# Kernel tuning notes

Hardware: AMD Instinct MI355X
Metric: run time of the kernel (lower is better)

## Reference

```python
import jax, jax.numpy as jnp
import numpy as np

D_MODEL = 1024
N_HEADS = 16
N_GROUPS = 4
D_FF = 4096
N_EXPERTS = 8
TOP_K = 2
BATCH = 2
SEQ = 1024
D_K = D_MODEL // N_HEADS
HPG = N_HEADS // N_GROUPS
EPS = 1e-6


def rms_norm(x, w):
    rms = jnp.sqrt(jnp.mean(x * x, axis=-1, keepdims=True) + EPS)
    return x / rms * w


def rope(x):
    # RoPE over FULL d_model, halves concatenated (faithful to source quirk)
    d = x.shape[-1]
    half = d // 2
    theta = 1.0 / (10000.0 ** (jnp.arange(half, dtype=jnp.float32) / half))
    pos = jnp.arange(x.shape[1], dtype=jnp.float32)[:, None]  # [S,1]
    ang = pos * theta[None, :]                                 # [S,half]
    cos, sin = jnp.cos(ang), jnp.sin(ang)
    xe, xo = x[..., 0::2], x[..., 1::2]
    return jnp.concatenate([xe * cos - xo * sin, xe * sin + xo * cos], axis=-1)


def attention(x, Wq, Wk, Wv, Wo):
    B, S, _ = x.shape
    xr = rope(x)
    Q = (xr @ Wq).reshape(B, S, N_HEADS, D_K).transpose(0, 2, 1, 3)  # [B,H,S,dk]
    Q = Q.reshape(B, N_GROUPS, HPG, S, D_K)
    K = (xr @ Wk).reshape(B, S, N_GROUPS, D_K).transpose(0, 2, 1, 3)  # [B,G,S,dk]
    V = (xr @ Wv).reshape(B, S, N_GROUPS, D_K).transpose(0, 2, 1, 3)
    scores = jnp.einsum('bghsd,bgtd->bghst', Q, K) / jnp.sqrt(jnp.float32(D_K))
    mask = jnp.triu(jnp.full((S, S), -1e9, dtype=scores.dtype), k=1)
    attn = jax.nn.softmax(scores + mask, axis=-1)
    out = jnp.einsum('bghst,bgtd->bghsd', attn, V)            # [B,G,Hg,S,dv]
    out = out.reshape(B, N_HEADS, S, D_K).transpose(0, 2, 1, 3).reshape(B, S, D_MODEL)
    return out @ Wo


def moe(x, router_w, router_b, W1, b1, W2, b2, W3, b3):
    B, S, _ = x.shape
    logits = x @ router_w + router_b                          # [B,S,E]
    topv, topi = jax.lax.top_k(logits, TOP_K)                 # [B,S,K]
    topw = jax.nn.softmax(topv, axis=-1)                      # [B,S,K]
    # scatter top-k weights into dense [B,S,E] combine matrix
    onehot = jax.nn.one_hot(topi, N_EXPERTS, dtype=x.dtype)   # [B,S,K,E]
    comb = jnp.einsum('bsk,bske->bse', topw, onehot)          # [B,S,E]
    # dense all-expert SwiGLU (same math as per-token dispatch loop)
    h1 = jnp.einsum('bsd,edf->ebsf', x, W1) + b1[:, None, None, :]
    h2 = jnp.einsum('bsd,edf->ebsf', x, W2) + b2[:, None, None, :]
    h = h2 * jax.nn.silu(h1)
    eo = jnp.einsum('ebsf,efd->ebsd', h, W3) + b3[:, None, None, :]
    return jnp.einsum('bse,ebsd->bsd', comb, eo)


def setup_inputs() -> dict:
    key = jax.random.key(0)
    ks = jax.random.split(key, 16)
    s = 0.02
    return {
        'x': jax.random.normal(ks[0], (BATCH, SEQ, D_MODEL), dtype=jnp.float32),
        'norm1_w': jnp.ones((D_MODEL,), jnp.float32),
        'Wq': jax.random.normal(ks[1], (D_MODEL, D_MODEL), jnp.float32) * s,
        'Wk': jax.random.normal(ks[2], (D_MODEL, N_GROUPS * D_K), jnp.float32) * s,
        'Wv': jax.random.normal(ks[3], (D_MODEL, N_GROUPS * D_K), jnp.float32) * s,
        'Wo': jax.random.normal(ks[4], (D_MODEL, D_MODEL), jnp.float32) * s,
        'norm2_w': jnp.ones((D_MODEL,), jnp.float32),
        'router_w': jax.random.normal(ks[5], (D_MODEL, N_EXPERTS), jnp.float32) * s,
        'router_b': jnp.zeros((N_EXPERTS,), jnp.float32),
        'W1': jax.random.normal(ks[6], (N_EXPERTS, D_MODEL, D_FF), jnp.float32) * s,
        'b1': jnp.zeros((N_EXPERTS, D_FF), jnp.float32),
        'W2': jax.random.normal(ks[7], (N_EXPERTS, D_MODEL, D_FF), jnp.float32) * s,
        'b2': jnp.zeros((N_EXPERTS, D_FF), jnp.float32),
        'W3': jax.random.normal(ks[8], (N_EXPERTS, D_FF, D_MODEL), jnp.float32) * s,
        'b3': jnp.zeros((N_EXPERTS, D_MODEL), jnp.float32),
    }


def reference(x, norm1_w, Wq, Wk, Wv, Wo, norm2_w, router_w, router_b,
              W1, b1, W2, b2, W3, b3):
    h = x + attention(rms_norm(x, norm1_w), Wq, Wk, Wv, Wo)
    h = h + moe(rms_norm(h, norm2_w), router_w, router_b, W1, b1, W2, b2, W3, b3)
    return h
```

## Files before the change

kernel.cpp:

```cpp
#include <hip/hip_runtime.h>

#define D_MODEL 1024
#define N_HEADS 16
#define N_GROUPS 4
#define D_FF 4096
#define N_EXPERTS 8
#define BATCH 2
#define SEQ 1024
#define DK 64
#define NTOK (BATCH*SEQ)
#define KVD (N_GROUPS*DK)
#define QKVN (D_MODEL + 2*KVD)
#define APAD 72

typedef unsigned short u16;
typedef unsigned int u32;
typedef __attribute__((ext_vector_type(8))) short short8;
typedef __attribute__((ext_vector_type(8))) __bf16 bf16x8;
typedef __attribute__((ext_vector_type(4))) float floatx4;

__device__ __forceinline__ float bf2f(u16 s){ return __uint_as_float(((u32)s)<<16); }
__device__ __forceinline__ u16 f2bf(float f){
  u32 u = __float_as_uint(f);
  u += 0x7fffu + ((u>>16)&1u);
  return (u16)(u>>16);
}
__device__ __forceinline__ floatx4 mfma16(short8 a, short8 b, floatx4 c){
  return __builtin_amdgcn_mfma_f32_16x16x32_bf16(
      __builtin_bit_cast(bf16x8, a), __builtin_bit_cast(bf16x8, b), c, 0, 0, 0);
}
__device__ __forceinline__ void gload16(const u16* g, u16* l){
  __builtin_amdgcn_global_load_lds(
      (const __attribute__((address_space(1))) u32*)g,
      (__attribute__((address_space(3))) u32*)l, 16, 0, 0);
}

__global__ __launch_bounds__(256) void k_cvt_t(
    const float* __restrict__ src, u16* __restrict__ dst, int K, int N)
{
  size_t moff = (size_t)blockIdx.z * K * N;
  src += moff; dst += moff;
  int k0 = blockIdx.y*64, n0 = blockIdx.x*64;
  __shared__ __align__(16) u16 t[64*72];
  int tid = threadIdx.x;
  #pragma unroll
  for (int i=0;i<4;i++){
    int idx = i*256 + tid;
    int r = idx>>4;
    int c = (idx&15)*4;
    float4 v = *(const float4*)(src + (size_t)(k0+r)*N + n0 + c);
    t[(c+0)*72 + r] = f2bf(v.x);
    t[(c+1)*72 + r] = f2bf(v.y);
    t[(c+2)*72 + r] = f2bf(v.z);
    t[(c+3)*72 + r] = f2bf(v.w);
  }
  __syncthreads();
  #pragma unroll
  for (int i=0;i<2;i++){
    int idx = i*256 + tid;
    int n = idx>>3;
    int kc = (idx&7)*8;
    *(uint4*)(dst + (size_t)(n0+n)*K + k0 + kc) = *(const uint4*)&t[n*72 + kc];
  }
}

__global__ __launch_bounds__(256) void k_rmsnorm_rope(
    const float* __restrict__ x, const float* __restrict__ w, u16* __restrict__ xr)
{
  int tok = blockIdx.x;
  int s = tok & (SEQ-1);
  int tid = threadIdx.x;
  const float* xrow = x + (size_t)tok * D_MODEL;
  __shared__ float red[256];
  float4 v = ((const float4*)xrow)[tid];
  red[tid] = v.x*v.x + v.y*v.y + v.z*v.z + v.w*v.w;
  __syncthreads();
  for (int o=128;o>0;o>>=1){ if(tid<o) red[tid]+=red[tid+o]; __syncthreads(); }
  float inv = rsqrtf(red[0]*(1.0f/D_MODEL) + 1e-6f);
  u16* orow = xr + (size_t)tok * D_MODEL;
  #pragma unroll
  for (int ii=0; ii<2; ii++){
    int i = tid + ii*256;
    float2 p = ((const float2*)xrow)[i];
    float2 wp = ((const float2*)w)[i];
    float xe = p.x*inv*wp.x;
    float xo = p.y*inv*wp.y;
    float th = __expf(-(float)i * (9.210340371976184f/512.0f));
    float ang = (float)s * th;
    float c = cosf(ang), sn = sinf(ang);
    orow[i]       = f2bf(xe*c - xo*sn);
    orow[i+512]   = f2bf(xe*sn + xo*c);
  }
}

__global__ __launch_bounds__(256) void k_gemm_t(
    const u16* __restrict__ A, const u16* __restrict__ Bt,
    u16* __restrict__ C, int M, int N, int K)
{
  __shared__ __align__(16) u16 As[2][64*32];
  __shared__ __align__(16) u16 Bs[2][128*32];
  int tid = threadIdx.x;
  int wave = tid>>6, lane = tid&63, l15 = lane&15, q = lane>>4;
  int wm = wave>>1, wn = wave&1;
  int m0 = blockIdx.y*64, n0 = blockIdx.x*128;
  const u16* ap  = A  + (size_t)(m0 + (tid>>2))*K + (tid&3)*8;
  const u16* bp0 = Bt + (size_t)(n0 + (tid>>2))*K + (tid&3)*8;
  const u16* bp1 = bp0 + (size_t)64*K;
  auto stage = [&](int buf, int k){
    gload16(ap  + k, &As[buf][wave*512]);
    gload16(bp0 + k, &Bs[buf][wave*512]);
    gload16(bp1 + k, &Bs[buf][2048 + wave*512]);
  };
  floatx4 acc[2][4];
  #pragma unroll
  for (int i=0;i<2;i++)
    #pragma unroll
    for (int j=0;j<4;j++) acc[i][j] = (floatx4){0.f,0.f,0.f,0.f};
  int NS = K/32, cur = 0;
  stage(0, 0);
  __syncthreads();
  for (int ks=0; ks<NS; ++ks){
    if (ks+1 < NS) stage(cur^1, (ks+1)*32);
    short8 af[2], bf[4];
    #pragma unroll
    for (int i=0;i<2;i++) af[i] = *(const short8*)&As[cur][(wm*32 + i*16 + l15)*32 + q*8];
    #pragma unroll
    for (int i=0;i<4;i++) bf[i] = *(const short8*)&Bs[cur][(wn*64 + i*16 + l15)*32 + q*8];
    #pragma unroll
    for (int mi=0;mi<2;mi++)
      #pragma unroll
      for (int ni=0;ni<4;ni++)
        acc[mi][ni] = mfma16(af[mi], bf[ni], acc[mi][ni]);
    __syncthreads();
    cur ^= 1;
  }
  #pragma unroll
  for (int mi=0;mi<2;mi++)
    #pragma unroll
    for (int ni=0;ni<4;ni++)
      #pragma unroll
      for (int r=0;r<4;r++){
        int row = m0 + wm*32 + mi*16 + q*4 + r;
        int col = n0 + wn*64 + ni*16 + l15;
        C[(size_t)row*N + col] = f2bf(acc[mi][ni][r]);
      }
}

__global__ __launch_bounds__(256) void k_gemm_resid(
    const u16* __restrict__ A, const u16* __restrict__ Bt,
    const float* __restrict__ resid, float* __restrict__ hacc,
    float* __restrict__ out, int M, int N, int K)
{
  __shared__ __align__(16) u16 As[2][64*32];
  __shared__ __align__(16) u16 Bs[2][128*32];
  int tid = threadIdx.x;
  int wave = tid>>6, lane = tid&63, l15 = lane&15, q = lane>>4;
  int wm = wave>>1, wn = wave&1;
  int m0 = blockIdx.y*64, n0 = blockIdx.x*128;
  const u16* ap  = A  + (size_t)(m0 + (tid>>2))*K + (tid&3)*8;
  const u16* bp0 = Bt + (size_t)(n0 + (tid>>2))*K + (tid&3)*8;
  const u16* bp1 = bp0 + (size_t)64*K;
  auto stage = [&](int buf, int k){
    gload16(ap  + k, &As[buf][wave*512]);
    gload16(bp0 + k, &Bs[buf][wave*512]);
    gload16(bp1 + k, &Bs[buf][2048 + wave*512]);
  };
  floatx4 acc[2][4];
  #pragma unroll
  for (int i=0;i<2;i++)
    #pragma unroll
    for (int j=0;j<4;j++) acc[i][j] = (floatx4){0.f,0.f,0.f,0.f};
  int NS = K/32, cur = 0;
  stage(0, 0);
  __syncthreads();
  for (int ks=0; ks<NS; ++ks){
    if (ks+1 < NS) stage(cur^1, (ks+1)*32);
    short8 af[2], bf[4];
    #pragma unroll
    for (int i=0;i<2;i++) af[i] = *(const short8*)&As[cur][(wm*32 + i*16 + l15)*32 + q*8];
    #pragma unroll
    for (int i=0;i<4;i++) bf[i] = *(const short8*)&Bs[cur][(wn*64 + i*16 + l15)*32 + q*8];
    #pragma unroll
    for (int mi=0;mi<2;mi++)
      #pragma unroll
      for (int ni=0;ni<4;ni++)
        acc[mi][ni] = mfma16(af[mi], bf[ni], acc[mi][ni]);
    __syncthreads();
    cur ^= 1;
  }
  #pragma unroll
  for (int mi=0;mi<2;mi++)
    #pragma unroll
    for (int ni=0;ni<4;ni++)
      #pragma unroll
      for (int r=0;r<4;r++){
        int row = m0 + wm*32 + mi*16 + q*4 + r;
        int col = n0 + wn*64 + ni*16 + l15;
        size_t idx = (size_t)row*N + col;
        float v = acc[mi][ni][r] + resid[idx];
        hacc[idx] = v;
        out[idx]  = v;
      }
}

__global__ __launch_bounds__(256) void k_vtrans(
    const u16* __restrict__ qkv, u16* __restrict__ Vt)
{
  int st = blockIdx.x;
  int bg = blockIdx.y;
  int b = bg >> 2, g = bg & 3;
  int tid = threadIdx.x;
  __shared__ u16 tile[64*APAD];
  #pragma unroll
  for (int i=0;i<2;i++){
    int idx = i*256 + tid;
    int srow = idx >> 3, cch = (idx&7)*8;
    uint4 v = *(const uint4*)(qkv + (size_t)(b*SEQ + st*64 + srow)*QKVN
                              + D_MODEL + KVD + g*64 + cch);
    *(uint4*)&tile[srow*APAD + cch] = v;
  }
  __syncthreads();
  #pragma unroll
  for (int i=0;i<2;i++){
    int idx = i*256 + tid;
    int drow = idx >> 3, sch = (idx&7)*8;
    u16 tmp[8];
    #pragma unroll
    for (int j=0;j<8;j++) tmp[j] = tile[(sch+j)*APAD + drow];
    *(uint4*)(Vt + ((size_t)(bg*64 + drow))*SEQ + st*64 + sch) = *(uint4*)tmp;
  }
}

__global__ __launch_bounds__(256) void k_attn_flash(
    const u16* __restrict__ qkv, const u16* __restrict__ Vt, u16* __restrict__ O)
{
  int qt = blockIdx.x, h = blockIdx.y, b = blockIdx.z;
  int g = h >> 2;
  int tid = threadIdx.x, wave = tid>>6, lane = tid&63, l15 = lane&15, q = lane>>4;
  __shared__ u16 Ks[64*APAD];
  __shared__ u16 Vs[64*APAD];
  __shared__ u16 Ps[4*16*APAD];

  int qbase = qt*64;
  const u16* qrow = qkv + (size_t)(b*SEQ + qbase + wave*16 + l15)*QKVN + h*64;
  short8 qa0 = *(const short8*)(qrow + q*8);
  short8 qa1 = *(const short8*)(qrow + 32 + q*8);

  floatx4 Of[4];
  #pragma unroll
  for (int nt=0;nt<4;nt++) Of[nt] = (floatx4){0.f,0.f,0.f,0.f};
  float mrun[4], lrun[4];
  #pragma unroll
  for (int r=0;r<4;r++){ mrun[r] = -1e30f; lrun[r] = 0.f; }

  for (int t=0; t<=qt; ++t){
    int kbase = t*64;
    __syncthreads();
    #pragma unroll
    for (int i=0;i<2;i++){
      int idx = i*256 + tid;
      int row = idx >> 3, cch = (idx&7)*8;
      uint4 kv = *(const uint4*)(qkv + (size_t)(b*SEQ + kbase + row)*QKVN
                                 + D_MODEL + g*64 + cch);
      *(uint4*)&Ks[row*APAD + cch] = kv;
      uint4 vv = *(const uint4*)(Vt + ((size_t)((b*4+g)*64 + row))*SEQ + kbase + cch);
      *(uint4*)&Vs[row*APAD + cch] = vv;
    }
    __syncthreads();

    floatx4 Sf[4];
    #pragma unroll
    for (int jt=0;jt<4;jt++){
      short8 bf0 = *(const short8*)&Ks[(jt*16+l15)*APAD + q*8];
      short8 bf1 = *(const short8*)&Ks[(jt*16+l15)*APAD + 32 + q*8];
      Sf[jt] = mfma16(qa0, bf0, (floatx4){0.f,0.f,0.f,0.f});
      Sf[jt] = mfma16(qa1, bf1, Sf[jt]);
    }
    bool maskt = (t == qt);
    #pragma unroll
    for (int r=0;r<4;r++){
      float s0 = Sf[0][r]*0.125f, s1 = Sf[1][r]*0.125f,
            s2 = Sf[2][r]*0.125f, s3 = Sf[3][r]*0.125f;
      if (maskt){
        int qg = qbase + wave*16 + q*4 + r;
        if (kbase +      l15 > qg) s0 = -1e30f;
        if (kbase + 16 + l15 > qg) s1 = -1e30f;
        if (kbase + 32 + l15 > qg) s2 = -1e30f;
        if (kbase + 48 + l15 > qg) s3 = -1e30f;
      }
      float mx = fmaxf(fmaxf(s0,s1), fmaxf(s2,s3));
      #pragma unroll
      for (int o=1;o<16;o<<=1) mx = fmaxf(mx, __shfl_xor(mx, o, 64));
      float mc = fmaxf(mrun[r], mx);
      float alpha = __expf(mrun[r]-mc);
      float p0 = __expf(s0-mc), p1 = __expf(s1-mc), p2 = __expf(s2-mc), p3 = __expf(s3-mc);
      float rs = p0+p1+p2+p3;
      #pragma unroll
      for (int o=1;o<16;o<<=1) rs += __shfl_xor(rs, o, 64);
      lrun[r] = lrun[r]*alpha + rs;
      mrun[r] = mc;
      #pragma unroll
      for (int nt=0;nt<4;nt++) Of[nt][r] *= alpha;
      int prow = wave*16*APAD + (q*4+r)*APAD;
      Ps[prow +      l15] = f2bf(p0);
      Ps[prow + 16 + l15] = f2bf(p1);
      Ps[prow + 32 + l15] = f2bf(p2);
      Ps[prow + 48 + l15] = f2bf(p3);
    }
    #pragma unroll
    for (int ks=0;ks<2;ks++){
      short8 pa = *(const short8*)&Ps[wave*16*APAD + l15*APAD + ks*32 + q*8];
      #pragma unroll
      for (int nt=0;nt<4;nt++){
        short8 vb = *(const short8*)&Vs[(nt*16+l15)*APAD + ks*32 + q*8];
        Of[nt] = mfma16(pa, vb, Of[nt]);
      }
    }
  }
  #pragma unroll
  for (int r=0;r<4;r++){
    float linv = 1.0f / lrun[r];
    int row = b*SEQ + qbase + wave*16 + q*4 + r;
    #pragma unroll
    for (int nt=0;nt<4;nt++){
      O[(size_t)row*D_MODEL + h*64 + nt*16 + l15] = f2bf(Of[nt][r]*linv);
    }
  }
}

__global__ __launch_bounds__(256) void k_rmsnorm2(
    const float* __restrict__ hacc, const float* __restrict__ w, u16* __restrict__ hn)
{
  int tok = blockIdx.x, tid = threadIdx.x;
  float4 v = ((const float4*)(hacc + (size_t)tok*D_MODEL))[tid];
  __shared__ float red[256];
  red[tid] = v.x*v.x + v.y*v.y + v.z*v.z + v.w*v.w;
  __syncthreads();
  for (int o=128;o>0;o>>=1){ if(tid<o) red[tid]+=red[tid+o]; __syncthreads(); }
  float inv = rsqrtf(red[0]*(1.0f/D_MODEL) + 1e-6f);
  int i = tid*4;
  float4 wv = ((const float4*)w)[tid];
  u16* orow = hn + (size_t)tok*D_MODEL;
  orow[i+0] = f2bf(v.x*inv*wv.x);
  orow[i+1] = f2bf(v.y*inv*wv.y);
  orow[i+2] = f2bf(v.z*inv*wv.z);
  orow[i+3] = f2bf(v.w*inv*wv.w);
}

__global__ __launch_bounds__(64) void k_router(
    const float* __restrict__ hacc, const float* __restrict__ w2,
    const float* __restrict__ rw, const float* __restrict__ rb,
    int* __restrict__ topi, float* __restrict__ topw)
{
  int tok = blockIdx.x, lane = threadIdx.x;
  const float* xrow = hacc + (size_t)tok*D_MODEL;
  float ss = 0.f;
  #pragma unroll
  for (int ii=0; ii<4; ii++){
    float4 v = ((const float4*)xrow)[lane + ii*64];
    ss += v.x*v.x + v.y*v.y + v.z*v.z + v.w*v.w;
  }
  #pragma unroll
  for (int o=32;o>0;o>>=1) ss += __shfl_down(ss, o, 64);
  ss = __shfl(ss, 0, 64);
  float inv = rsqrtf(ss*(1.0f/D_MODEL) + 1e-6f);
  float accv[8] = {0.f,0.f,0.f,0.f,0.f,0.f,0.f,0.f};
  for (int d = lane; d < D_MODEL; d += 64){
    float xv = xrow[d]*inv*w2[d];
    float4 r0 = ((const float4*)(rw + (size_t)d*8))[0];
    float4 r1 = ((const float4*)(rw + (size_t)d*8))[1];
    accv[0] += xv*r0.x; accv[1] += xv*r0.y;
    accv[2] += xv*r0.z; accv[3] += xv*r0.w;
    accv[4] += xv*r1.x; accv[5] += xv*r1.y;
    accv[6] += xv*r1.z; accv[7] += xv*r1.w;
  }
  #pragma unroll
  for (int e=0;e<8;e++){
    #pragma unroll
    for (int o=32;o>0;o>>=1) accv[e] += __shfl_down(accv[e], o, 64);
  }
  if (lane==0){
    float lg[8];
    #pragma unroll
    for (int e=0;e<8;e++) lg[e] = accv[e] + rb[e];
    int i0=0; float v0=lg[0];
    for (int e=1;e<8;e++) if (lg[e]>v0){v0=lg[e]; i0=e;}
    int i1=-1; float v1=-1e30f;
    for (int e=0;e<8;e++) if (e!=i0 && lg[e]>v1){v1=lg[e]; i1=e;}
    float e1 = __expf(v1-v0);
    float wsum = 1.f + e1;
    topi[tok*2+0]=i0; topi[tok*2+1]=i1;
    topw[tok*2+0]=1.f/wsum; topw[tok*2+1]=e1/wsum;
  }
}

__global__ __launch_bounds__(256) void k_pack(
    const int* __restrict__ topi, const float* __restrict__ topw,
    int* __restrict__ off, int* __restrict__ perm, float* __restrict__ pw)
{
  __shared__ int cnt[8], cur[8], offs[9];
  int tid = threadIdx.x;
  if (tid<8) cnt[tid]=0;
  __syncthreads();
  for (int i=tid;i<NTOK*2;i+=256) atomicAdd(&cnt[topi[i]],1);
  __syncthreads();
  if (tid==0){
    int s=0;
    for (int e=0;e<8;e++){ offs[e]=s; s+=cnt[e]; }
    offs[8]=s;
    for (int e=0;e<9;e++) off[e]=offs[e];
  }
  __syncthreads();
  if (tid<8) cur[tid]=offs[tid];
  __syncthreads();
  for (int i=tid;i<NTOK*2;i+=256){
    int e = topi[i];
    int pos = atomicAdd(&cur[e],1);
    perm[pos] = i>>1;
    pw[pos]   = topw[i];
  }
}

__global__ __launch_bounds__(256) void k_moe1(
    const u16* __restrict__ hn,
    const u16* __restrict__ W1t, const float* __restrict__ b1,
    const u16* __restrict__ W2t, const float* __restrict__ b2,
    const int* __restrict__ off, const int* __restrict__ perm,
    u16* __restrict__ H)
{
  int e = blockIdx.z;
  int base = off[e], cnte = off[e+1]-base;
  int mt = blockIdx.y;
  if (mt*128 >= cnte) return;
  int n0 = blockIdx.x*64;
  __shared__ __align__(16) u16 As[2][128*32];
  __shared__ __align__(16) u16 B1s[2][64*32];
  __shared__ __align__(16) u16 B2s[2][64*32];
  int tid = threadIdx.x;
  int wave = tid>>6, lane = tid&63, l15 = lane&15, q = lane>>4;
  int wm = wave>>1, wn = wave&1;
  int r0 = mt*128 + (tid>>2), r1 = r0 + 64;
  int t0 = (r0 < cnte) ? perm[base+r0] : 0;
  int t1 = (r1 < cnte) ? perm[base+r1] : 0;
  const u16* ap0 = hn + (size_t)t0*D_MODEL + (tid&3)*8;
  const u16* ap1 = hn + (size_t)t1*D_MODEL + (tid&3)*8;
  const u16* b1p = W1t + (size_t)e*D_FF*D_MODEL + (size_t)(n0 + (tid>>2))*D_MODEL + (tid&3)*8;
  const u16* b2p = W2t + (size_t)e*D_FF*D_MODEL + (size_t)(n0 + (tid>>2))*D_MODEL + (tid&3)*8;
  auto stage = [&](int buf, int k){
    gload16(ap0 + k, &As[buf][wave*512]);
    gload16(ap1 + k, &As[buf][2048 + wave*512]);
    gload16(b1p + k, &B1s[buf][wave*512]);
    gload16(b2p + k, &B2s[buf][wave*512]);
  };
  floatx4 acc1[4][2], acc2[4][2];
  #pragma unroll
  for (int i=0;i<4;i++)
    #pragma unroll
    for (int j=0;j<2;j++){ acc1[i][j]=(floatx4){0.f,0.f,0.f,0.f}; acc2[i][j]=(floatx4){0.f,0.f,0.f,0.f}; }
  int cur = 0;
  stage(0, 0);
  __syncthreads();
  for (int ks=0; ks<D_MODEL/32; ++ks){
    if (ks+1 < D_MODEL/32) stage(cur^1, (ks+1)*32);
    short8 af[4], f1[2], f2[2];
    #pragma unroll
    for (int i=0;i<4;i++) af[i] = *(const short8*)&As[cur][(wm*64 + i*16 + l15)*32 + q*8];
    #pragma unroll
    for (int i=0;i<2;i++){
      f1[i] = *(const short8*)&B1s[cur][(wn*32 + i*16 + l15)*32 + q*8];
      f2[i] = *(const short8*)&B2s[cur][(wn*32 + i*16 + l15)*32 + q*8];
    }
    #pragma unroll
    for (int mi=0;mi<4;mi++)
      #pragma unroll
      for (int ni=0;ni<2;ni++){
        acc1[mi][ni] = mfma16(af[mi], f1[ni], acc1[mi][ni]);
        acc2[mi][ni] = mfma16(af[mi], f2[ni], acc2[mi][ni]);
      }
    __syncthreads();
    cur ^= 1;
  }
  #pragma unroll
  for (int mi=0;mi<4;mi++)
    #pragma unroll
    for (int ni=0;ni<2;ni++)
      #pragma unroll
      for (int r=0;r<4;r++){
        int rloc = wm*64 + mi*16 + q*4 + r;
        int grow = mt*128 + rloc;
        if (grow < cnte){
          int col = n0 + wn*32 + ni*16 + l15;
          float h1 = acc1[mi][ni][r] + b1[e*D_FF+col];
          float h2 = acc2[mi][ni][r] + b2[e*D_FF+col];
          float sil = h1 / (1.f + __expf(-h1));
          H[(size_t)(base + grow)*D_FF + col] = f2bf(h2*sil);
        }
      }
}

__global__ __launch_bounds__(256) void k_moe2(
    const u16* __restrict__ H, const u16* __restrict__ W3t, const float* __restrict__ b3,
    const int* __restrict__ off, const int* __restrict__ perm, const float* __restrict__ pw,
    float* __restrict__ out)
{
  int e = blockIdx.z;
  int base = off[e], cnte = off[e+1]-base;
  int mt = blockIdx.y >> 1;
  int ksp = blockIdx.y & 1;
  if (mt*64 >= cnte) return;
  int n0 = blockIdx.x*128;
  __shared__ __align__(16) u16 As[2][64*32];
  __shared__ __align__(16) u16 Bs[2][128*32];
  int tid = threadIdx.x;
  int wave = tid>>6, lane = tid&63, l15 = lane&15, q = lane>>4;
  int wm = wave>>1, wn = wave&1;
  const u16* ap  = H + (size_t)(base + mt*64 + (tid>>2))*D_FF + ksp*2048 + (tid&3)*8;
  const u16* bp0 = W3t + (size_t)e*D_MODEL*D_FF + (size_t)(n0 + (tid>>2))*D_FF + ksp*2048 + (tid&3)*8;
  const u16* bp1 = bp0 + (size_t)64*D_FF;
  auto stage = [&](int buf, int k){
    gload16(ap  + k, &As[buf][wave*512]);
    gload16(bp0 + k, &Bs[buf][wave*512]);
    gload16(bp1 + k, &Bs[buf][2048 + wave*512]);
  };
  floatx4 acc[2][4];
  #pragma unroll
  for (int i=0;i<2;i++)
    #pragma unroll
    for (int j=0;j<4;j++) acc[i][j] = (floatx4){0.f,0.f,0.f,0.f};
  int cur = 0;
  stage(0, 0);
  __syncthreads();
  for (int ks=0; ks<64; ++ks){
    if (ks+1 < 64) stage(cur^1, (ks+1)*32);
    short8 af[2], bf[4];
    #pragma unroll
    for (int i=0;i<2;i++) af[i] = *(const short8*)&As[cur][(wm*32 + i*16 + l15)*32 + q*8];
    #pragma unroll
    for (int i=0;i<4;i++) bf[i] = *(const short8*)&Bs[cur][(wn*64 + i*16 + l15)*32 + q*8];
    #pragma unroll
    for (int mi=0;mi<2;mi++)
      #pragma unroll
      for (int ni=0;ni<4;ni++)
        acc[mi][ni] = mfma16(af[mi], bf[ni], acc[mi][ni]);
    __syncthreads();
    cur ^= 1;
  }
  #pragma unroll
  for (int mi=0;mi<2;mi++)
    #pragma unroll
    for (int ni=0;ni<4;ni++)
      #pragma unroll
      for (int r=0;r<4;r++){
        int grow = mt*64 + wm*32 + mi*16 + q*4 + r;
        if (grow < cnte){
          int col = n0 + wn*64 + ni*16 + l15;
          int tok = perm[base+grow];
          float wgt = pw[base+grow];
          float val = acc[mi][ni][r] + (ksp==0 ? b3[e*D_MODEL+col] : 0.f);
          atomicAdd(out + (size_t)tok*D_MODEL + col, wgt*val);
        }
      }
}

extern "C" void kernel_launch(void* const* d_in, const int* in_sizes, int n_in,
                              void* d_out, int out_size, void* d_ws, size_t ws_size,
                              hipStream_t stream)
{
  const float* x   = (const float*)d_in[0];
  const float* n1w = (const float*)d_in[1];
  const float* Wq  = (const float*)d_in[2];
  const float* Wk  = (const float*)d_in[3];
  const float* Wv  = (const float*)d_in[4];
  const float* Wo  = (const float*)d_in[5];
  const float* n2w = (const float*)d_in[6];
  const float* rw  = (const float*)d_in[7];
  const float* rb  = (const float*)d_in[8];
  const float* W1  = (const float*)d_in[9];
  const float* b1  = (const float*)d_in[10];
  const float* W2  = (const float*)d_in[11];
  const float* b2  = (const float*)d_in[12];
  const float* W3  = (const float*)d_in[13];
  const float* b3  = (const float*)d_in[14];
  float* out = (float*)d_out;

  char* p = (char*)d_ws;
  auto alloc = [&](size_t bytes)->char*{
    char* r = p; p += (bytes + 255) & ~(size_t)255; return r;
  };
  u16*   xr   = (u16*)  alloc((size_t)NTOK*D_MODEL*2);
  u16*   qkv  = (u16*)  alloc((size_t)NTOK*QKVN*2);
  u16*   Vt   = (u16*)  alloc((size_t)NTOK*KVD*2);
  u16*   attn = (u16*)  alloc((size_t)NTOK*D_MODEL*2);
  u16*   hn   = (u16*)  alloc((size_t)NTOK*D_MODEL*2);
  float* acc  = (float*)alloc((size_t)NTOK*D_MODEL*4);
  int*   topi = (int*)  alloc((size_t)NTOK*2*4);
  float* topw = (float*)alloc((size_t)NTOK*2*4);
  int*   off  = (int*)  alloc(64);
  int*   perm = (int*)  alloc((size_t)NTOK*2*4);
  float* pw   = (float*)alloc((size_t)NTOK*2*4);
  u16*   H    = (u16*)  alloc((size_t)NTOK*2*D_FF*2);
  u16*   Wqkvt= (u16*)  alloc((size_t)QKVN*D_MODEL*2);
  u16*   Wot  = (u16*)  alloc((size_t)D_MODEL*D_MODEL*2);
  u16*   W1t  = (u16*)  alloc((size_t)N_EXPERTS*D_MODEL*D_FF*2);
  u16*   W2t  = (u16*)  alloc((size_t)N_EXPERTS*D_MODEL*D_FF*2);
  u16*   W3t  = (u16*)  alloc((size_t)N_EXPERTS*D_FF*D_MODEL*2);

  k_cvt_t<<<dim3(D_MODEL/64, D_MODEL/64, 1), 256, 0, stream>>>(Wq, Wqkvt, D_MODEL, D_MODEL);
  k_cvt_t<<<dim3(KVD/64,     D_MODEL/64, 1), 256, 0, stream>>>(Wk, Wqkvt + (size_t)D_MODEL*D_MODEL, D_MODEL, KVD);
  k_cvt_t<<<dim3(KVD/64,     D_MODEL/64, 1), 256, 0, stream>>>(Wv, Wqkvt + (size_t)(D_MODEL+KVD)*D_MODEL, D_MODEL, KVD);
  k_cvt_t<<<dim3(D_MODEL/64, D_MODEL/64, 1), 256, 0, stream>>>(Wo, Wot, D_MODEL, D_MODEL);
  k_cvt_t<<<dim3(D_FF/64,    D_MODEL/64, N_EXPERTS), 256, 0, stream>>>(W1, W1t, D_MODEL, D_FF);
  k_cvt_t<<<dim3(D_FF/64,    D_MODEL/64, N_EXPERTS), 256, 0, stream>>>(W2, W2t, D_MODEL, D_FF);
  k_cvt_t<<<dim3(D_MODEL/64, D_FF/64,    N_EXPERTS), 256, 0, stream>>>(W3, W3t, D_FF, D_MODEL);

  k_rmsnorm_rope<<<NTOK, 256, 0, stream>>>(x, n1w, xr);
  k_gemm_t<<<dim3(QKVN/128, NTOK/64), 256, 0, stream>>>(xr, Wqkvt, qkv, NTOK, QKVN, D_MODEL);
  k_vtrans<<<dim3(SEQ/64, BATCH*N_GROUPS), 256, 0, stream>>>(qkv, Vt);
  k_attn_flash<<<dim3(SEQ/64, N_HEADS, BATCH), 256, 0, stream>>>(qkv, Vt, attn);
  k_gemm_resid<<<dim3(D_MODEL/128, NTOK/64), 256, 0, stream>>>(attn, Wot, x, acc, out, NTOK, D_MODEL, D_MODEL);
  k_rmsnorm2<<<NTOK, 256, 0, stream>>>(acc, n2w, hn);
  k_router<<<NTOK, 64, 0, stream>>>(acc, n2w, rw, rb, topi, topw);
  k_pack<<<1, 256, 0, stream>>>(topi, topw, off, perm, pw);
  k_moe1<<<dim3(D_FF/64,     32, N_EXPERTS), 256, 0, stream>>>(hn, W1t, b1, W2t, b2, off, perm, H);
  k_moe2<<<dim3(D_MODEL/128, 128, N_EXPERTS), 256, 0, stream>>>(H, W3t, b3, off, perm, pw, out);
}
```

Before: 786.8 us.

## Drop LDS double buffering and load A fragments directly from global memory

The GEMM kernels stop double-buffering in LDS. k_gemm_t, k_gemm_resid and k_moe1 now read A-operand MFMA fragments straight from global memory into registers, and only B tiles are staged through a single LDS buffer with two barriers per k-step. k_moe2 keeps staging both A and B but in single buffers, and clamps out-of-range A rows so it no longer reads past valid rows. This cuts LDS use and may raise occupancy, but it drops the overlap of the next tile's load with the current MFMAs and adds uncoalesced global reads for A, so load latency is exposed.

```diff
diff --git a/kernel.cpp b/kernel.cpp
--- a/kernel.cpp
+++ b/kernel.cpp
@@ -97,42 +97,37 @@
     const u16* __restrict__ A, const u16* __restrict__ Bt,
     u16* __restrict__ C, int M, int N, int K)
 {
-  __shared__ __align__(16) u16 As[2][64*32];
-  __shared__ __align__(16) u16 Bs[2][128*32];
+  __shared__ __align__(16) u16 Bs[128*32];
   int tid = threadIdx.x;
   int wave = tid>>6, lane = tid&63, l15 = lane&15, q = lane>>4;
   int wm = wave>>1, wn = wave&1;
   int m0 = blockIdx.y*64, n0 = blockIdx.x*128;
-  const u16* ap  = A  + (size_t)(m0 + (tid>>2))*K + (tid&3)*8;
+  const u16* arow[2];
+  #pragma unroll
+  for (int i=0;i<2;i++)
+    arow[i] = A + (size_t)(m0 + wm*32 + i*16 + l15)*K + q*8;
   const u16* bp0 = Bt + (size_t)(n0 + (tid>>2))*K + (tid&3)*8;
   const u16* bp1 = bp0 + (size_t)64*K;
-  auto stage = [&](int buf, int k){
-    gload16(ap  + k, &As[buf][wave*512]);
-    gload16(bp0 + k, &Bs[buf][wave*512]);
-    gload16(bp1 + k, &Bs[buf][2048 + wave*512]);
-  };
   floatx4 acc[2][4];
   #pragma unroll
   for (int i=0;i<2;i++)
     #pragma unroll
     for (int j=0;j<4;j++) acc[i][j] = (floatx4){0.f,0.f,0.f,0.f};
-  int NS = K/32, cur = 0;
-  stage(0, 0);
-  __syncthreads();
-  for (int ks=0; ks<NS; ++ks){
-    if (ks+1 < NS) stage(cur^1, (ks+1)*32);
+  for (int k0=0;k0<K;k0+=32){
+    __syncthreads();
+    gload16(bp0 + k0, &Bs[wave*512]);
+    gload16(bp1 + k0, &Bs[2048 + wave*512]);
+    __syncthreads();
     short8 af[2], bf[4];
     #pragma unroll
-    for (int i=0;i<2;i++) af[i] = *(const short8*)&As[cur][(wm*32 + i*16 + l15)*32 + q*8];
-    #pragma unroll
-    for (int i=0;i<4;i++) bf[i] = *(const short8*)&Bs[cur][(wn*64 + i*16 + l15)*32 + q*8];
+    for (int i=0;i<2;i++) af[i] = *(const short8*)(arow[i] + k0);
+    #pragma unroll
+    for (int i=0;i<4;i++) bf[i] = *(const short8*)&Bs[(wn*64 + i*16 + l15)*32 + q*8];
     #pragma unroll
     for (int mi=0;mi<2;mi++)
       #pragma unroll
       for (int ni=0;ni<4;ni++)
         acc[mi][ni] = mfma16(af[mi], bf[ni], acc[mi][ni]);
-    __syncthreads();
-    cur ^= 1;
   }
   #pragma unroll
   for (int mi=0;mi<2;mi++)
@@ -151,42 +146,37 @@
     const float* __restrict__ resid, float* __restrict__ hacc,
     float* __restrict__ out, int M, int N, int K)
 {
-  __shared__ __align__(16) u16 As[2][64*32];
-  __shared__ __align__(16) u16 Bs[2][128*32];
+  __shared__ __align__(16) u16 Bs[128*32];
   int tid = threadIdx.x;
   int wave = tid>>6, lane = tid&63, l15 = lane&15, q = lane>>4;
   int wm = wave>>1, wn = wave&1;
   int m0 = blockIdx.y*64, n0 = blockIdx.x*128;
-  const u16* ap  = A  + (size_t)(m0 + (tid>>2))*K + (tid&3)*8;
+  const u16* arow[2];
+  #pragma unroll
+  for (int i=0;i<2;i++)
+    arow[i] = A + (size_t)(m0 + wm*32 + i*16 + l15)*K + q*8;
   const u16* bp0 = Bt + (size_t)(n0 + (tid>>2))*K + (tid&3)*8;
   const u16* bp1 = bp0 + (size_t)64*K;
-  auto stage = [&](int buf, int k){
-    gload16(ap  + k, &As[buf][wave*512]);
-    gload16(bp0 + k, &Bs[buf][wave*512]);
-    gload16(bp1 + k, &Bs[buf][2048 + wave*512]);
-  };
   floatx4 acc[2][4];
   #pragma unroll
   for (int i=0;i<2;i++)
     #pragma unroll
     for (int j=0;j<4;j++) acc[i][j] = (floatx4){0.f,0.f,0.f,0.f};
-  int NS = K/32, cur = 0;
-  stage(0, 0);
-  __syncthreads();
-  for (int ks=0; ks<NS; ++ks){
-    if (ks+1 < NS) stage(cur^1, (ks+1)*32);
+  for (int k0=0;k0<K;k0+=32){
+    __syncthreads();
+    gload16(bp0 + k0, &Bs[wave*512]);
+    gload16(bp1 + k0, &Bs[2048 + wave*512]);
+    __syncthreads();
     short8 af[2], bf[4];
     #pragma unroll
-    for (int i=0;i<2;i++) af[i] = *(const short8*)&As[cur][(wm*32 + i*16 + l15)*32 + q*8];
-    #pragma unroll
-    for (int i=0;i<4;i++) bf[i] = *(const short8*)&Bs[cur][(wn*64 + i*16 + l15)*32 + q*8];
+    for (int i=0;i<2;i++) af[i] = *(const short8*)(arow[i] + k0);
+    #pragma unroll
+    for (int i=0;i<4;i++) bf[i] = *(const short8*)&Bs[(wn*64 + i*16 + l15)*32 + q*8];
     #pragma unroll
     for (int mi=0;mi<2;mi++)
       #pragma unroll
       for (int ni=0;ni<4;ni++)
         acc[mi][ni] = mfma16(af[mi], bf[ni], acc[mi][ni]);
-    __syncthreads();
-    cur ^= 1;
   }
   #pragma unroll
   for (int mi=0;mi<2;mi++)
@@ -433,42 +423,37 @@
   int mt = blockIdx.y;
   if (mt*128 >= cnte) return;
   int n0 = blockIdx.x*64;
-  __shared__ __align__(16) u16 As[2][128*32];
-  __shared__ __align__(16) u16 B1s[2][64*32];
-  __shared__ __align__(16) u16 B2s[2][64*32];
+  __shared__ __align__(16) u16 B1s[64*32];
+  __shared__ __align__(16) u16 B2s[64*32];
   int tid = threadIdx.x;
   int wave = tid>>6, lane = tid&63, l15 = lane&15, q = lane>>4;
   int wm = wave>>1, wn = wave&1;
-  int r0 = mt*128 + (tid>>2), r1 = r0 + 64;
-  int t0 = (r0 < cnte) ? perm[base+r0] : 0;
-  int t1 = (r1 < cnte) ? perm[base+r1] : 0;
-  const u16* ap0 = hn + (size_t)t0*D_MODEL + (tid&3)*8;
-  const u16* ap1 = hn + (size_t)t1*D_MODEL + (tid&3)*8;
+  const u16* arow[4];
+  #pragma unroll
+  for (int i=0;i<4;i++){
+    int grow = mt*128 + wm*64 + i*16 + l15;
+    int t = (grow < cnte) ? perm[base+grow] : 0;
+    arow[i] = hn + (size_t)t*D_MODEL + q*8;
+  }
   const u16* b1p = W1t + (size_t)e*D_FF*D_MODEL + (size_t)(n0 + (tid>>2))*D_MODEL + (tid&3)*8;
   const u16* b2p = W2t + (size_t)e*D_FF*D_MODEL + (size_t)(n0 + (tid>>2))*D_MODEL + (tid&3)*8;
-  auto stage = [&](int buf, int k){
-    gload16(ap0 + k, &As[buf][wave*512]);
-    gload16(ap1 + k, &As[buf][2048 + wave*512]);
-    gload16(b1p + k, &B1s[buf][wave*512]);
-    gload16(b2p + k, &B2s[buf][wave*512]);
-  };
   floatx4 acc1[4][2], acc2[4][2];
   #pragma unroll
   for (int i=0;i<4;i++)
     #pragma unroll
     for (int j=0;j<2;j++){ acc1[i][j]=(floatx4){0.f,0.f,0.f,0.f}; acc2[i][j]=(floatx4){0.f,0.f,0.f,0.f}; }
-  int cur = 0;
-  stage(0, 0);
-  __syncthreads();
-  for (int ks=0; ks<D_MODEL/32; ++ks){
-    if (ks+1 < D_MODEL/32) stage(cur^1, (ks+1)*32);
+  for (int k0=0;k0<D_MODEL;k0+=32){
+    __syncthreads();
+    gload16(b1p + k0, &B1s[wave*512]);
+    gload16(b2p + k0, &B2s[wave*512]);
+    __syncthreads();
     short8 af[4], f1[2], f2[2];
     #pragma unroll
-    for (int i=0;i<4;i++) af[i] = *(const short8*)&As[cur][(wm*64 + i*16 + l15)*32 + q*8];
+    for (int i=0;i<4;i++) af[i] = *(const short8*)(arow[i] + k0);
     #pragma unroll
     for (int i=0;i<2;i++){
-      f1[i] = *(const short8*)&B1s[cur][(wn*32 + i*16 + l15)*32 + q*8];
-      f2[i] = *(const short8*)&B2s[cur][(wn*32 + i*16 + l15)*32 + q*8];
+      f1[i] = *(const short8*)&B1s[(wn*32 + i*16 + l15)*32 + q*8];
+      f2[i] = *(const short8*)&B2s[(wn*32 + i*16 + l15)*32 + q*8];
     }
     #pragma unroll
     for (int mi=0;mi<4;mi++)
@@ -477,8 +462,6 @@
         acc1[mi][ni] = mfma16(af[mi], f1[ni], acc1[mi][ni]);
         acc2[mi][ni] = mfma16(af[mi], f2[ni], acc2[mi][ni]);
       }
-    __syncthreads();
-    cur ^= 1;
   }
   #pragma unroll
   for (int mi=0;mi<4;mi++)
@@ -509,41 +492,38 @@
   int ksp = blockIdx.y & 1;
   if (mt*64 >= cnte) return;
   int n0 = blockIdx.x*128;
-  __shared__ __align__(16) u16 As[2][64*32];
-  __shared__ __align__(16) u16 Bs[2][128*32];
+  __shared__ __align__(16) u16 As[64*32];
+  __shared__ __align__(16) u16 Bs[128*32];
   int tid = threadIdx.x;
   int wave = tid>>6, lane = tid&63, l15 = lane&15, q = lane>>4;
   int wm = wave>>1, wn = wave&1;
-  const u16* ap  = H + (size_t)(base + mt*64 + (tid>>2))*D_FF + ksp*2048 + (tid&3)*8;
+  int arr = mt*64 + (tid>>2);
+  if (arr >= cnte) arr = cnte-1;
+  const u16* ap  = H + (size_t)(base + arr)*D_FF + ksp*2048 + (tid&3)*8;
   const u16* bp0 = W3t + (size_t)e*D_MODEL*D_FF + (size_t)(n0 + (tid>>2))*D_FF + ksp*2048 + (tid&3)*8;
   const u16* bp1 = bp0 + (size_t)64*D_FF;
-  auto stage = [&](int buf, int k){
-    gload16(ap  + k, &As[buf][wave*512]);
-    gload16(bp0 + k, &Bs[buf][wave*512]);
-    gload16(bp1 + k, &Bs[buf][2048 + wave*512]);
-  };
   floatx4 acc[2][4];
   #pragma unroll
   for (int i=0;i<2;i++)
     #pragma unroll
     for (int j=0;j<4;j++) acc[i][j] = (floatx4){0.f,0.f,0.f,0.f};
-  int cur = 0;
-  stage(0, 0);
-  __syncthreads();
   for (int ks=0; ks<64; ++ks){
-    if (ks+1 < 64) stage(cur^1, (ks+1)*32);
+    int k0 = ks*32;
+    __syncthreads();
+    gload16(ap  + k0, &As[wave*512]);
+    gload16(bp0 + k0, &Bs[wave*512]);
+    gload16(bp1 + k0, &Bs[2048 + wave*512]);
+    __syncthreads();
     short8 af[2], bf[4];
     #pragma unroll
-    for (int i=0;i<2;i++) af[i] = *(const short8*)&As[cur][(wm*32 + i*16 + l15)*32 + q*8];
-    #pragma unroll
-    for (int i=0;i<4;i++) bf[i] = *(const short8*)&Bs[cur][(wn*64 + i*16 + l15)*32 + q*8];
+    for (int i=0;i<2;i++) af[i] = *(const short8*)&As[(wm*32 + i*16 + l15)*32 + q*8];
+    #pragma unroll
+    for (int i=0;i<4;i++) bf[i] = *(const short8*)&Bs[(wn*64 + i*16 + l15)*32 + q*8];
     #pragma unroll
     for (int mi=0;mi<2;mi++)
       #pragma unroll
       for (int ni=0;ni<4;ni++)
         acc[mi][ni] = mfma16(af[mi], bf[ni], acc[mi][ni]);
-    __syncthreads();
-    cur ^= 1;
   }
   #pragma unroll
   for (int mi=0;mi<2;mi++)
```

Result: slower. 876.9 us (+11.5%).
